# Optimization experiments

Measured on AMD Instinct MI355X. Metric: run time of the kernel, lower is better.

## Reference

```python
import jax, jax.numpy as jnp
import numpy as np

# Model dims (match init_kwargs)
E = 512        # embed_dim
H = 8          # n_heads
L = 6          # n_layers
DFF = 2048     # PyTorch TransformerEncoderLayer default dim_feedforward
K = 1024       # codebook_size
V = 32         # num_joints
NQ = 1         # n_q
T = 64         # frames
B = 2
MAX_T = 512    # time_pos table size
LN_EPS = 1e-5


def make_block_causal_mask(t, v):
    """True=keep. Causal across frames, full attention within a frame."""
    s = t * v
    i = np.arange(s)
    tril = i[:, None] >= i[None, :]
    same_frame = (i[:, None] // v) == (i[None, :] // v)
    return jnp.asarray(tril | same_frame)


def setup_inputs() -> dict:
    key = jax.random.key(0)
    ks = jax.random.split(key, 20)
    sc = 0.02
    inp = {
        "indices": jax.random.randint(ks[0], (B, T, V, NQ), 0, K, dtype=jnp.int64 if jax.config.jax_enable_x64 else jnp.int32),
        "attention_mask": make_block_causal_mask(T, V),
        # embedding tables
        "code_emb": jax.random.normal(ks[1], (K, E), jnp.float32) * sc,
        "stage_emb": jax.random.normal(ks[2], (NQ, E), jnp.float32) * sc,
        "time_pos": jax.random.normal(ks[3], (MAX_T, E), jnp.float32) * sc,
        "joint_pos": jax.random.normal(ks[4], (V, E), jnp.float32) * sc,
        # per-layer stacked transformer params
        "in_proj_w": jax.random.normal(ks[5], (L, 3 * E, E), jnp.float32) * sc,
        "in_proj_b": jnp.zeros((L, 3 * E), jnp.float32),
        "out_w": jax.random.normal(ks[6], (L, E, E), jnp.float32) * sc,
        "out_b": jnp.zeros((L, E), jnp.float32),
        "ln1_g": jnp.ones((L, E), jnp.float32),
        "ln1_b": jnp.zeros((L, E), jnp.float32),
        "lin1_w": jax.random.normal(ks[7], (L, DFF, E), jnp.float32) * sc,
        "lin1_b": jnp.zeros((L, DFF), jnp.float32),
        "lin2_w": jax.random.normal(ks[8], (L, E, DFF), jnp.float32) * sc,
        "lin2_b": jnp.zeros((L, E), jnp.float32),
        "ln2_g": jnp.ones((L, E), jnp.float32),
        "ln2_b": jnp.zeros((L, E), jnp.float32),
    }
    return inp


def _ln(x, g, b):
    mu = jnp.mean(x, axis=-1, keepdims=True)
    var = jnp.mean(jnp.square(x - mu), axis=-1, keepdims=True)
    return (x - mu) * jax.lax.rsqrt(var + LN_EPS) * g + b


def _mha(x, keep, wi, bi, wo, bo):
    Bq, S, _ = x.shape
    dh = E // H
    qkv = x @ wi.T + bi                       # [B,S,3E]
    q, k, v = jnp.split(qkv, 3, axis=-1)
    q = q.reshape(Bq, S, H, dh)
    k = k.reshape(Bq, S, H, dh)
    v = v.reshape(Bq, S, H, dh)
    scores = jnp.einsum('bqhd,bkhd->bhqk', q, k) / jnp.sqrt(jnp.float32(dh))
    scores = jnp.where(keep[None, None], scores, jnp.float32(-1e30))
    attn = jax.nn.softmax(scores, axis=-1)
    o = jnp.einsum('bhqk,bkhd->bqhd', attn, v).reshape(Bq, S, E)
    return o @ wo.T + bo


def _transformer(indices, keep, code_emb, stage_emb, time_pos, joint_pos,
                 in_proj_w, in_proj_b, out_w, out_b, ln1_g, ln1_b,
                 lin1_w, lin1_b, lin2_w, lin2_b, ln2_g, ln2_b):
    Bq, Tq, Vq, nq = indices.shape
    emb = code_emb[indices] + stage_emb[None, None, None]       # [B,T,V,nq,E]
    emb = emb.reshape(Bq, Tq, Vq * nq, E)
    v_ids = jnp.repeat(jnp.arange(Vq), nq)
    emb = emb + time_pos[:Tq][None, :, None, :] + joint_pos[v_ids][None, None, :, :]
    x = emb.reshape(Bq, Tq * Vq * nq, E)
    for l in range(L):
        y = _ln(x, ln1_g[l], ln1_b[l])
        x = x + _mha(y, keep, in_proj_w[l], in_proj_b[l], out_w[l], out_b[l])
        y = _ln(x, ln2_g[l], ln2_b[l])
        h = jax.nn.gelu(y @ lin1_w[l].T + lin1_b[l], approximate=False)
        x = x + h @ lin2_w[l].T + lin2_b[l]
    return x.reshape(Bq, Tq, Vq * nq, E)


def reference(indices, attention_mask, code_emb, stage_emb, time_pos, joint_pos,
              in_proj_w, in_proj_b, out_w, out_b, ln1_g, ln1_b,
              lin1_w, lin1_b, lin2_w, lin2_b, ln2_g, ln2_b):
    # attention_mask is [T*V, T*V] with n_q=1, so no repeat_interleave needed.
    keep = attention_mask
    if NQ > 1 and attention_mask.shape[0] == T * V:
        keep = jnp.repeat(jnp.repeat(attention_mask, NQ, 0), NQ, 1)
    return _transformer(indices, keep, code_emb, stage_emb, time_pos, joint_pos,
                        in_proj_w, in_proj_b, out_w, out_b, ln1_g, ln1_b,
                        lin1_w, lin1_b, lin2_w, lin2_b, ln2_g, ln2_b)
```

## Files before the change

kernel.cpp:

```cpp
#include <hip/hip_runtime.h>
#include <hip/hip_bf16.h>
#include <math.h>

#define E 512
#define H_HEADS 8
#define DH 64
#define NLAYER 6
#define DFF 2048
#define SEQ 2048
#define NB 2
#define M_TOK (NB*SEQ)

typedef float f32x4_t __attribute__((ext_vector_type(4)));
typedef __bf16 bf16x8_t __attribute__((ext_vector_type(8)));
typedef short s16x8_t __attribute__((ext_vector_type(8)));

__device__ __forceinline__ short f2bf(float f) {
    union { float f; unsigned u; } v; v.f = f;
    unsigned r = v.u + 0x7FFFu + ((v.u >> 16) & 1u);
    return (short)(r >> 16);
}

__device__ __forceinline__ bf16x8_t mk_frag(short4 lo, short4 hi) {
    s16x8_t t;
    t[0] = lo.x; t[1] = lo.y; t[2] = lo.z; t[3] = lo.w;
    t[4] = hi.x; t[5] = hi.y; t[6] = hi.z; t[7] = hi.w;
    return __builtin_bit_cast(bf16x8_t, t);
}

__device__ __forceinline__ void gload16(const void* g, void* l) {
    __builtin_amdgcn_global_load_lds(
        (const __attribute__((address_space(1))) void*)g,
        (__attribute__((address_space(3))) void*)l, 16, 0, 0);
}

__global__ __launch_bounds__(256) void embed_kernel(
    const int* __restrict__ idx, const float* __restrict__ ce,
    const float* __restrict__ se, const float* __restrict__ tp,
    const float* __restrict__ jp, float* __restrict__ x)
{
    int i = blockIdx.x * 256 + threadIdx.x;
    int e4 = i & 127;
    int row = i >> 7;
    int v = row & 31;
    int t = (row >> 5) & 63;
    int code = idx[row];
    const float4* ce4 = (const float4*)ce;
    const float4* se4 = (const float4*)se;
    const float4* tp4 = (const float4*)tp;
    const float4* jp4 = (const float4*)jp;
    float4 a = ce4[code * 128 + e4];
    float4 b = se4[e4];
    float4 c = tp4[t * 128 + e4];
    float4 d = jp4[v * 128 + e4];
    float4 o;
    o.x = a.x + b.x + c.x + d.x;
    o.y = a.y + b.y + c.y + d.y;
    o.z = a.z + b.z + c.z + d.z;
    o.w = a.w + b.w + c.w + d.w;
    ((float4*)x)[i] = o;
}

__global__ __launch_bounds__(256) void cast4_kernel(
    const float* __restrict__ w0, const float* __restrict__ w1,
    const float* __restrict__ w2, const float* __restrict__ w3,
    short* __restrict__ o)
{
    int i = blockIdx.x * 256 + threadIdx.x;
    const float* src; int off;
    if (i < 98304)       { src = w0; off = i; }
    else if (i < 131072) { src = w1; off = i - 98304; }
    else if (i < 262144) { src = w2; off = i - 131072; }
    else                 { src = w3; off = i - 262144; }
    float4 a = ((const float4*)src)[off * 2];
    float4 b = ((const float4*)src)[off * 2 + 1];
    s16x8_t s;
    s[0] = f2bf(a.x); s[1] = f2bf(a.y); s[2] = f2bf(a.z); s[3] = f2bf(a.w);
    s[4] = f2bf(b.x); s[5] = f2bf(b.y); s[6] = f2bf(b.z); s[7] = f2bf(b.w);
    *(s16x8_t*)&o[(size_t)i * 8] = s;
}

__global__ __launch_bounds__(256) void ln_kernel(
    const float* __restrict__ x, short* __restrict__ y,
    const float* __restrict__ g, const float* __restrict__ b)
{
    int wave = threadIdx.x >> 6;
    int lane = threadIdx.x & 63;
    int row = blockIdx.x * 4 + wave;
    const float4* xr = (const float4*)(x + (size_t)row * E);
    float4 v0 = xr[lane];
    float4 v1 = xr[lane + 64];
    float s  = v0.x + v0.y + v0.z + v0.w + v1.x + v1.y + v1.z + v1.w;
    float ss = v0.x*v0.x + v0.y*v0.y + v0.z*v0.z + v0.w*v0.w
             + v1.x*v1.x + v1.y*v1.y + v1.z*v1.z + v1.w*v1.w;
    #pragma unroll
    for (int off = 32; off; off >>= 1) {
        s  += __shfl_xor(s, off, 64);
        ss += __shfl_xor(ss, off, 64);
    }
    float mu = s * (1.f / E);
    float var = ss * (1.f / E) - mu * mu;
    float rs = rsqrtf(var + 1e-5f);
    const float4* g4 = (const float4*)g;
    const float4* b4 = (const float4*)b;
    float4 gg = g4[lane], bb = b4[lane];
    short4 o;
    o.x = f2bf((v0.x - mu) * rs * gg.x + bb.x);
    o.y = f2bf((v0.y - mu) * rs * gg.y + bb.y);
    o.z = f2bf((v0.z - mu) * rs * gg.z + bb.z);
    o.w = f2bf((v0.w - mu) * rs * gg.w + bb.w);
    *(short4*)&y[(size_t)row * E + lane * 4] = o;
    gg = g4[lane + 64]; bb = b4[lane + 64];
    o.x = f2bf((v1.x - mu) * rs * gg.x + bb.x);
    o.y = f2bf((v1.y - mu) * rs * gg.y + bb.y);
    o.z = f2bf((v1.z - mu) * rs * gg.z + bb.z);
    o.w = f2bf((v1.w - mu) * rs * gg.w + bb.w);
    *(short4*)&y[(size_t)row * E + 256 + lane * 4] = o;
}

template<int MODE>
__global__ __launch_bounds__(256) void gemm_mfma_kernel(
    const short* __restrict__ A, const short* __restrict__ W,
    const float* __restrict__ bias, const float* __restrict__ res,
    void* __restrict__ out, int N, int K)
{
    __shared__ short As[128 * 64];
    __shared__ short Bs[128 * 64];
    int nb = N >> 7;
    int bx = blockIdx.x % nb;
    int by = blockIdx.x / nb;
    int tid = threadIdx.x;
    int lane = tid & 63, g = lane >> 4, l16 = lane & 15;
    int w = tid >> 6, wm = w >> 1, wn = w & 1;
    int wbase = tid & 192;

    f32x4_t acc[4][4] = {};
    const short* Ab = A + (size_t)(by * 128) * K;
    const short* Wb = W + (size_t)(bx * 128) * K;

    for (int k0 = 0; k0 < K; k0 += 64) {
        __syncthreads();
        #pragma unroll
        for (int u = 0; u < 4; ++u) {
            int c = u * 256 + tid;
            int row = c >> 3, c8 = c & 7;
            gload16(Ab + (size_t)row * K + k0 + c8 * 8, As + (u * 256 + wbase) * 8);
            gload16(Wb + (size_t)row * K + k0 + c8 * 8, Bs + (u * 256 + wbase) * 8);
        }
        __syncthreads();
        #pragma unroll
        for (int ks = 0; ks < 2; ++ks) {
            bf16x8_t af[4], bf[4];
            #pragma unroll
            for (int i = 0; i < 4; ++i) {
                af[i] = *(const bf16x8_t*)&As[(wm * 64 + i * 16 + l16) * 64 + ks * 32 + g * 8];
                bf[i] = *(const bf16x8_t*)&Bs[(wn * 64 + i * 16 + l16) * 64 + ks * 32 + g * 8];
            }
            #pragma unroll
            for (int mi = 0; mi < 4; ++mi)
                #pragma unroll
                for (int ni = 0; ni < 4; ++ni)
                    acc[mi][ni] = __builtin_amdgcn_mfma_f32_16x16x32_bf16(
                        af[mi], bf[ni], acc[mi][ni], 0, 0, 0);
        }
    }

    int gm0 = by * 128 + wm * 64;
    int gn0 = bx * 128 + wn * 64;
    #pragma unroll
    for (int ni = 0; ni < 4; ++ni) {
        int gn = gn0 + ni * 16 + l16;
        float bv = bias[gn];
        #pragma unroll
        for (int mi = 0; mi < 4; ++mi) {
            #pragma unroll
            for (int r = 0; r < 4; ++r) {
                int gm = gm0 + mi * 16 + g * 4 + r;
                float v = acc[mi][ni][r] + bv;
                if (MODE == 2) v = 0.5f * v * (1.f + erff(v * 0.70710678118f));
                if (MODE == 1) {
                    v += res[(size_t)gm * N + gn];
                    ((float*)out)[(size_t)gm * N + gn] = v;
                } else {
                    ((short*)out)[(size_t)gm * N + gn] = f2bf(v);
                }
            }
        }
    }
}

__global__ __launch_bounds__(128) void attn_mfma_kernel(
    const short* __restrict__ qkv, short* __restrict__ out)
{
    __shared__ __align__(16) short Qs[32 * 68];
    __shared__ __align__(16) short Ks[32 * 68];
    __shared__ __align__(16) short Vt[64 * 36];
    __shared__ __align__(16) float Ol[2 * 16 * 68];

    int bid = blockIdx.x;
    int qb = 63 - (bid & 63);
    int h  = (bid >> 6) & 7;
    int b  = bid >> 9;
    int tid  = threadIdx.x;
    int w    = tid >> 6;
    int lane = tid & 63;
    int g    = lane >> 4;
    int l16  = lane & 15;

    const short* base = qkv + (size_t)(b * SEQ) * 1536;

    #pragma unroll
    for (int u = 0; u < 4; ++u) {
        int f = tid + 128 * u;
        int qr = f >> 4, c4 = f & 15;
        short4 v = *(const short4*)(base + (size_t)(qb * 32 + qr) * 1536 + h * 64 + c4 * 4);
        *(short4*)&Qs[qr * 68 + c4 * 4] = v;
    }

    int kend = (qb + 1) * 32;
    short4 kreg[4], vreg[4];
    #pragma unroll
    for (int u = 0; u < 4; ++u) {
        int f = tid + 128 * u;
        int key = f >> 4, c4 = f & 15;
        const short* row = base + (size_t)key * 1536 + h * 64;
        kreg[u] = *(const short4*)(row + 512 + c4 * 4);
        vreg[u] = *(const short4*)(row + 1024 + c4 * 4);
    }
    __syncthreads();

    bf16x8_t qf[2];
    #pragma unroll
    for (int ks = 0; ks < 2; ++ks) {
        const short* qrow = &Qs[(w * 16 + l16) * 68];
        short4 lo = *(const short4*)&qrow[4 * g + 32 * ks];
        short4 hi = *(const short4*)&qrow[4 * g + 16 + 32 * ks];
        qf[ks] = mk_frag(lo, hi);
    }

    f32x4_t oa[4] = {};
    float mrun = -1e30f, lrun = 0.f;

    for (int kt = 0; kt < kend; kt += 32) {
        __syncthreads();
        #pragma unroll
        for (int u = 0; u < 4; ++u) {
            int f = tid + 128 * u;
            int key = f >> 4, c4 = f & 15;
            *(short4*)&Ks[key * 68 + c4 * 4] = kreg[u];
            Vt[(c4 * 4 + 0) * 36 + key] = vreg[u].x;
            Vt[(c4 * 4 + 1) * 36 + key] = vreg[u].y;
            Vt[(c4 * 4 + 2) * 36 + key] = vreg[u].z;
            Vt[(c4 * 4 + 3) * 36 + key] = vreg[u].w;
        }
        if (kt + 32 < kend) {
            #pragma unroll
            for (int u = 0; u < 4; ++u) {
                int f = tid + 128 * u;
                int key = f >> 4, c4 = f & 15;
                const short* row = base + (size_t)(kt + 32 + key) * 1536 + h * 64;
                kreg[u] = *(const short4*)(row + 512 + c4 * 4);
                vreg[u] = *(const short4*)(row + 1024 + c4 * 4);
            }
        }
        __syncthreads();

        f32x4_t st[2];
        __builtin_amdgcn_s_setprio(1);
        #pragma unroll
        for (int mt = 0; mt < 2; ++mt) {
            f32x4_t acc = {0.f, 0.f, 0.f, 0.f};
            #pragma unroll
            for (int ks = 0; ks < 2; ++ks) {
                const short* krow = &Ks[(mt * 16 + l16) * 68];
                short4 lo = *(const short4*)&krow[4 * g + 32 * ks];
                short4 hi = *(const short4*)&krow[4 * g + 16 + 32 * ks];
                acc = __builtin_amdgcn_mfma_f32_16x16x32_bf16(mk_frag(lo, hi), qf[ks], acc, 0, 0, 0);
            }
            st[mt] = acc;
        }
        __builtin_amdgcn_s_setprio(0);

        float s8[8];
        #pragma unroll
        for (int mt = 0; mt < 2; ++mt)
            #pragma unroll
            for (int r = 0; r < 4; ++r)
                s8[mt * 4 + r] = st[mt][r] * 0.125f;
        float tm = s8[0];
        #pragma unroll
        for (int j = 1; j < 8; ++j) tm = fmaxf(tm, s8[j]);
        tm = fmaxf(tm, __shfl_xor(tm, 16));
        tm = fmaxf(tm, __shfl_xor(tm, 32));
        float mnew = fmaxf(mrun, tm);
        float c = __expf(mrun - mnew);
        mrun = mnew;
        float ps = 0.f;
        short pb[8];
        #pragma unroll
        for (int j = 0; j < 8; ++j) {
            float p = __expf(s8[j] - mrun);
            ps += p;
            pb[j] = f2bf(p);
        }
        ps += __shfl_xor(ps, 16);
        ps += __shfl_xor(ps, 32);
        lrun = lrun * c + ps;
        #pragma unroll
        for (int dt = 0; dt < 4; ++dt)
            #pragma unroll
            for (int r = 0; r < 4; ++r)
                oa[dt][r] *= c;
        s16x8_t pt;
        #pragma unroll
        for (int j = 0; j < 8; ++j) pt[j] = pb[j];
        bf16x8_t pf = __builtin_bit_cast(bf16x8_t, pt);

        __builtin_amdgcn_s_setprio(1);
        #pragma unroll
        for (int dt = 0; dt < 4; ++dt) {
            const short* vrow = &Vt[(dt * 16 + l16) * 36];
            short4 lo = *(const short4*)&vrow[4 * g];
            short4 hi = *(const short4*)&vrow[16 + 4 * g];
            oa[dt] = __builtin_amdgcn_mfma_f32_16x16x32_bf16(mk_frag(lo, hi), pf, oa[dt], 0, 0, 0);
        }
        __builtin_amdgcn_s_setprio(0);
    }

    float inv = 1.f / lrun;
    #pragma unroll
    for (int dt = 0; dt < 4; ++dt)
        #pragma unroll
        for (int r = 0; r < 4; ++r)
            Ol[(w * 16 + l16) * 68 + 16 * dt + 4 * g + r] = oa[dt][r] * inv;
    int qr = lane >> 2, cc = lane & 3;
    const float* orow = &Ol[(w * 16 + qr) * 68 + cc * 16];
    s16x8_t s0, s1;
    #pragma unroll
    for (int j = 0; j < 8; ++j) { s0[j] = f2bf(orow[j]); s1[j] = f2bf(orow[8 + j]); }
    size_t gb = (size_t)(b * SEQ + qb * 32 + w * 16 + qr) * E + h * 64 + cc * 16;
    *(s16x8_t*)&out[gb] = s0;
    *(s16x8_t*)&out[gb + 8] = s1;
}

extern "C" void kernel_launch(void* const* d_in, const int* in_sizes, int n_in,
                              void* d_out, int out_size, void* d_ws, size_t ws_size,
                              hipStream_t stream) {
    const int*   idx = (const int*)d_in[0];
    const float* ce  = (const float*)d_in[2];
    const float* se  = (const float*)d_in[3];
    const float* tp  = (const float*)d_in[4];
    const float* jp  = (const float*)d_in[5];
    const float* ipw = (const float*)d_in[6];
    const float* ipb = (const float*)d_in[7];
    const float* ow  = (const float*)d_in[8];
    const float* ob  = (const float*)d_in[9];
    const float* l1g = (const float*)d_in[10];
    const float* l1b = (const float*)d_in[11];
    const float* w1  = (const float*)d_in[12];
    const float* b1  = (const float*)d_in[13];
    const float* w2  = (const float*)d_in[14];
    const float* b2  = (const float*)d_in[15];
    const float* l2g = (const float*)d_in[16];
    const float* l2b = (const float*)d_in[17];

    float* x = (float*)d_out;
    short* y_bf   = (short*)d_ws;
    short* qkv_bf = (short*)((char*)d_ws + (4u << 20));
    short* h_bf   = qkv_bf;
    short* wb     = (short*)((char*)d_ws + (20u << 20));
    short* wip = wb;
    short* wob = wb + 786432;
    short* w1b = wb + 1048576;
    short* w2b = wb + 2097152;

    embed_kernel<<<2048, 256, 0, stream>>>(idx, ce, se, tp, jp, x);

    for (int l = 0; l < NLAYER; ++l) {
        cast4_kernel<<<1536, 256, 0, stream>>>(
            ipw + (size_t)l * 786432, ow + (size_t)l * 262144,
            w1 + (size_t)l * 1048576, w2 + (size_t)l * 1048576, wb);
        ln_kernel<<<1024, 256, 0, stream>>>(x, y_bf, l1g + l * E, l1b + l * E);
        gemm_mfma_kernel<0><<<32 * 12, 256, 0, stream>>>(
            y_bf, wip, ipb + (size_t)l * 1536, nullptr, qkv_bf, 1536, 512);
        attn_mfma_kernel<<<1024, 128, 0, stream>>>(qkv_bf, y_bf);
        gemm_mfma_kernel<1><<<32 * 4, 256, 0, stream>>>(
            y_bf, wob, ob + (size_t)l * E, x, x, 512, 512);
        ln_kernel<<<1024, 256, 0, stream>>>(x, y_bf, l2g + l * E, l2b + l * E);
        gemm_mfma_kernel<2><<<32 * 16, 256, 0, stream>>>(
            y_bf, w1b, b1 + (size_t)l * DFF, nullptr, h_bf, 2048, 512);
        gemm_mfma_kernel<1><<<32 * 4, 256, 0, stream>>>(
            h_bf, w2b, b2 + (size_t)l * E, x, x, 512, 2048);
    }
}
```

Before: 1.231 ms.

## Split causal attention along keys into chunks with a separate combine kernel

Attention work for each query block is split into up to four key chunks of 512 keys, each run by its own block. Each block writes unnormalized partial outputs in bf16 plus running max and sum, and a new combine kernel merges them with log-sum-exp rescaling. The intent is to balance the triangular causal workload, where late query blocks walked up to 2048 keys serially, and to give the GPU more parallel blocks. The cost is an extra kernel launch, extra global traffic for partial results, and some rounding from storing partials in bf16. Shared memory is also reused through a union to cut its footprint.

After: 1.225 ms. Within noise of the previous version (-0.4%).

```diff
diff --git a/kernel.cpp b/kernel.cpp
--- a/kernel.cpp
+++ b/kernel.cpp
@@ -19,6 +19,10 @@
     union { float f; unsigned u; } v; v.f = f;
     unsigned r = v.u + 0x7FFFu + ((v.u >> 16) & 1u);
     return (short)(r >> 16);
+}
+__device__ __forceinline__ float bf2f(short s) {
+    union { unsigned u; float f; } v; v.u = ((unsigned)(unsigned short)s) << 16;
+    return v.f;
 }
 
 __device__ __forceinline__ bf16x8_t mk_frag(short4 lo, short4 hi) {
@@ -190,17 +194,24 @@
 }
 
 __global__ __launch_bounds__(128) void attn_mfma_kernel(
-    const short* __restrict__ qkv, short* __restrict__ out)
-{
-    __shared__ __align__(16) short Qs[32 * 68];
-    __shared__ __align__(16) short Ks[32 * 68];
-    __shared__ __align__(16) short Vt[64 * 36];
-    __shared__ __align__(16) float Ol[2 * 16 * 68];
+    const short* __restrict__ qkv, short* __restrict__ opart,
+    float* __restrict__ mlbuf)
+{
+    __shared__ __align__(16) char smem[13312];
+    short* Qs = (short*)smem;
+    short* Ks = (short*)(smem + 4352);
+    short* Vt = (short*)(smem + 8704);
+    float* Ol = (float*)smem;
 
     int bid = blockIdx.x;
-    int qb = 63 - (bid & 63);
-    int h  = (bid >> 6) & 7;
-    int b  = bid >> 9;
+    int c   = bid & 3;
+    int qb  = 63 - ((bid >> 2) & 63);
+    int bh  = bid >> 8;
+    if (c * 16 > qb) return;
+    int h = bh & 7, b = bh >> 3;
+    int a_ = qb >> 4, r_ = qb & 15;
+    int cidx = bh * 160 + (a_ + 1) * (8 * a_ + r_) + c;
+
     int tid  = threadIdx.x;
     int w    = tid >> 6;
     int lane = tid & 63;
@@ -217,13 +228,15 @@
         *(short4*)&Qs[qr * 68 + c4 * 4] = v;
     }
 
-    int kend = (qb + 1) * 32;
+    int kstart = c * 512;
+    int kcend  = min((qb + 1) * 32, kstart + 512);
+
     short4 kreg[4], vreg[4];
     #pragma unroll
     for (int u = 0; u < 4; ++u) {
         int f = tid + 128 * u;
         int key = f >> 4, c4 = f & 15;
-        const short* row = base + (size_t)key * 1536 + h * 64;
+        const short* row = base + (size_t)(kstart + key) * 1536 + h * 64;
         kreg[u] = *(const short4*)(row + 512 + c4 * 4);
         vreg[u] = *(const short4*)(row + 1024 + c4 * 4);
     }
@@ -241,7 +254,7 @@
     f32x4_t oa[4] = {};
     float mrun = -1e30f, lrun = 0.f;
 
-    for (int kt = 0; kt < kend; kt += 32) {
+    for (int kt = kstart; kt < kcend; kt += 32) {
         __syncthreads();
         #pragma unroll
         for (int u = 0; u < 4; ++u) {
@@ -253,7 +266,7 @@
             Vt[(c4 * 4 + 2) * 36 + key] = vreg[u].z;
             Vt[(c4 * 4 + 3) * 36 + key] = vreg[u].w;
         }
-        if (kt + 32 < kend) {
+        if (kt + 32 < kcend) {
             #pragma unroll
             for (int u = 0; u < 4; ++u) {
                 int f = tid + 128 * u;
@@ -293,7 +306,7 @@
         tm = fmaxf(tm, __shfl_xor(tm, 16));
         tm = fmaxf(tm, __shfl_xor(tm, 32));
         float mnew = fmaxf(mrun, tm);
-        float c = __expf(mrun - mnew);
+        float cf = __expf(mrun - mnew);
         mrun = mnew;
         float ps = 0.f;
         short pb[8];
@@ -305,12 +318,12 @@
         }
         ps += __shfl_xor(ps, 16);
         ps += __shfl_xor(ps, 32);
-        lrun = lrun * c + ps;
+        lrun = lrun * cf + ps;
         #pragma unroll
         for (int dt = 0; dt < 4; ++dt)
             #pragma unroll
             for (int r = 0; r < 4; ++r)
-                oa[dt][r] *= c;
+                oa[dt][r] *= cf;
         s16x8_t pt;
         #pragma unroll
         for (int j = 0; j < 8; ++j) pt[j] = pb[j];
@@ -327,20 +340,69 @@
         __builtin_amdgcn_s_setprio(0);
     }
 
-    float inv = 1.f / lrun;
+    __syncthreads();
     #pragma unroll
     for (int dt = 0; dt < 4; ++dt)
         #pragma unroll
         for (int r = 0; r < 4; ++r)
-            Ol[(w * 16 + l16) * 68 + 16 * dt + 4 * g + r] = oa[dt][r] * inv;
-    int qr = lane >> 2, cc = lane & 3;
-    const float* orow = &Ol[(w * 16 + qr) * 68 + cc * 16];
+            Ol[(w * 16 + l16) * 68 + 16 * dt + 4 * g + r] = oa[dt][r];
+    if (g == 0) {
+        mlbuf[cidx * 64 + w * 16 + l16] = mrun;
+        mlbuf[cidx * 64 + 32 + w * 16 + l16] = lrun;
+    }
+    int q = tid >> 2, d0 = (tid & 3) * 16;
+    const float* orow = &Ol[q * 68 + d0];
     s16x8_t s0, s1;
     #pragma unroll
     for (int j = 0; j < 8; ++j) { s0[j] = f2bf(orow[j]); s1[j] = f2bf(orow[8 + j]); }
-    size_t gb = (size_t)(b * SEQ + qb * 32 + w * 16 + qr) * E + h * 64 + cc * 16;
-    *(s16x8_t*)&out[gb] = s0;
-    *(s16x8_t*)&out[gb + 8] = s1;
+    size_t ob = (size_t)cidx * 2048 + q * 64 + d0;
+    *(s16x8_t*)&opart[ob] = s0;
+    *(s16x8_t*)&opart[ob + 8] = s1;
+}
+
+__global__ __launch_bounds__(128) void attn_combine_kernel(
+    const short* __restrict__ opart, const float* __restrict__ mlbuf,
+    short* __restrict__ y)
+{
+    int bid = blockIdx.x;
+    int qb = bid & 63, bh = bid >> 6;
+    int h = bh & 7, b = bh >> 3;
+    int a_ = qb >> 4, r_ = qb & 15;
+    int cbase = bh * 160 + (a_ + 1) * (8 * a_ + r_);
+    int nc = a_ + 1;
+    int t = threadIdx.x;
+    int q = t >> 2, d0 = (t & 3) * 16;
+
+    float M = -1e30f;
+    #pragma unroll
+    for (int cc = 0; cc < 4; ++cc)
+        if (cc < nc) M = fmaxf(M, mlbuf[(cbase + cc) * 64 + q]);
+    float L = 0.f;
+    float acc[16] = {};
+    #pragma unroll
+    for (int cc = 0; cc < 4; ++cc) {
+        if (cc < nc) {
+            float mv = mlbuf[(cbase + cc) * 64 + q];
+            float lv = mlbuf[(cbase + cc) * 64 + 32 + q];
+            float wgt = __expf(mv - M);
+            L += wgt * lv;
+            const short* op = &opart[(size_t)(cbase + cc) * 2048 + q * 64 + d0];
+            s16x8_t v0 = *(const s16x8_t*)op;
+            s16x8_t v1 = *(const s16x8_t*)(op + 8);
+            #pragma unroll
+            for (int j = 0; j < 8; ++j) {
+                acc[j]     += wgt * bf2f(v0[j]);
+                acc[8 + j] += wgt * bf2f(v1[j]);
+            }
+        }
+    }
+    float inv = 1.f / L;
+    s16x8_t o0, o1;
+    #pragma unroll
+    for (int j = 0; j < 8; ++j) { o0[j] = f2bf(acc[j] * inv); o1[j] = f2bf(acc[8 + j] * inv); }
+    size_t gb = (size_t)(b * SEQ + qb * 32 + q) * E + h * 64 + d0;
+    *(s16x8_t*)&y[gb] = o0;
+    *(s16x8_t*)&y[gb + 8] = o1;
 }
 
 extern "C" void kernel_launch(void* const* d_in, const int* in_sizes, int n_in,
@@ -373,6 +435,8 @@
     short* wob = wb + 786432;
     short* w1b = wb + 1048576;
     short* w2b = wb + 2097152;
+    short* opart = (short*)((char*)d_ws + (27u << 20));
+    float* mlbuf = (float*)((char*)d_ws + (37u << 20));
 
     embed_kernel<<<2048, 256, 0, stream>>>(idx, ce, se, tp, jp, x);
 
@@ -383,7 +447,8 @@
         ln_kernel<<<1024, 256, 0, stream>>>(x, y_bf, l1g + l * E, l1b + l * E);
         gemm_mfma_kernel<0><<<32 * 12, 256, 0, stream>>>(
             y_bf, wip, ipb + (size_t)l * 1536, nullptr, qkv_bf, 1536, 512);
-        attn_mfma_kernel<<<1024, 128, 0, stream>>>(qkv_bf, y_bf);
+        attn_mfma_kernel<<<4096, 128, 0, stream>>>(qkv_bf, opart, mlbuf);
+        attn_combine_kernel<<<1024, 128, 0, stream>>>(opart, mlbuf, y_bf);
         gemm_mfma_kernel<1><<<32 * 4, 256, 0, stream>>>(
             y_bf, wob, ob + (size_t)l * E, x, x, 512, 512);
         ln_kernel<<<1024, 256, 0, stream>>>(x, y_bf, l2g + l * E, l2b + l * E);
```
